# Kernel tuning notes

Hardware: AMD Instinct MI355X
Metric: run time of the kernel (lower is better)

Reference implementation:

```python
import jax, jax.numpy as jnp
import numpy as np

_N = 262144  # horizon
_n = 64      # state dim
_m = 32      # observation dim


def setup_inputs() -> dict:
    key = jax.random.key(0)
    k1, k2, k3, k4 = jax.random.split(key, 4)
    # Scale so the closed-loop matrix M = A - L H is stable (spectral radius < 1);
    # otherwise the 262k-step recurrence overflows fp32.
    A = jax.random.normal(k1, (_n, _n), jnp.float32) * (0.7 / np.sqrt(_n))
    H = jax.random.normal(k2, (_m, _n), jnp.float32) * (1.0 / np.sqrt(_n))
    L = jax.random.normal(k3, (_n, _m), jnp.float32) * (0.1 / np.sqrt(_m))
    y = jax.random.normal(k4, (_m, _N), jnp.float32)
    return {"y": y, "A": A, "H": H, "L": L, "N": _N}


def reference(y, A, H, L, N):
    # xhat[k+1] = A xhat[k] + L (y[:,k] - H xhat[:,k]) = (A - L H) xhat[k] + L y[:,k]
    # yhat[:,k] = H xhat[:,k],  xhat[0] = 0
    M = A - L @ H  # (n, n) closed-loop transition
    x0 = jnp.zeros((A.shape[0],), dtype=A.dtype)

    def step(x, yk):
        yhat_k = H @ x          # emitted BEFORE the update (matches loop order)
        x_next = M @ x + L @ yk
        return x_next, yhat_k

    _, yhat = jax.lax.scan(step, x0, y.T[:N])  # yhat: (N, m)
    return yhat.T  # (m, N)
```

## Files before the change

### kernel.cpp

```cpp
#include <hip/hip_runtime.h>
#include <hip/hip_bf16.h>


#define NSTEP 262144
#define T 16
#define CCH (NSTEP / T)
#define KDIM (64 + 32 * T)
#define MOUT (32 * T)
#define NBLK 128
#define SB (CCH / NBLK)

typedef _Float16 f16;
typedef _Float16 f16x4 __attribute__((ext_vector_type(4)));
typedef _Float16 f16x8 __attribute__((ext_vector_type(8)));
typedef float f32x4 __attribute__((ext_vector_type(4)));


#define OFF_ZH 0
#define SZ_ZH  (CCH * KDIM / 2)
#define OFF_VT (OFF_ZH + SZ_ZH)
#define SZ_VT  (CCH * 64)
#define OFF_MP (OFF_VT + SZ_VT)
#define SZ_MP  (8 * 4096)
#define OFF_BO (OFF_MP + SZ_MP)
#define SZ_BO  (MOUT * KDIM / 2)
#define OFF_GC (OFF_BO + SZ_BO)
#define SZ_GC  (64 * 512 / 2)
#define OFF_FB (OFF_GC + SZ_GC)
#define SZ_FB  (16 * 2048)
#define OFF_GB (OFF_FB + SZ_FB)
#define SZ_GB  (16 * 2048)
#define OFF_KD (OFF_GB + SZ_GB)
#define SZ_KD  (15 * 1024)
#define OFF_W  (OFF_KD + SZ_KD)
#define OFF_XB (OFF_W + NBLK * 64)

__global__ __launch_bounds__(256) void k_pack(const float* __restrict__ y,
                                              f16* __restrict__ Zt) {
  __shared__ f16 Lt[32][264];
  const int tid = threadIdx.x;
  const int ct = blockIdx.x;
  const size_t colbase = (size_t)ct * 256;
#pragma unroll
  for (int v = 0; v < 8; ++v) {
    const int fidx = v * 256 + tid;
    const int row = fidx >> 6, col4 = fidx & 63;
    const float4 w = *reinterpret_cast<const float4*>(y + (size_t)row * NSTEP + colbase + col4 * 4);
    f16x4 h = {(f16)w.x, (f16)w.y, (f16)w.z, (f16)w.w};
    *reinterpret_cast<f16x4*>(&Lt[row][col4 * 4]) = h;
  }
  __syncthreads();
#pragma unroll
  for (int v = 0; v < 4; ++v) {
    const int s = v * 256 + tid;
    const int l = s & 15, lg = (s >> 4) & 3, t = s >> 6;
    f16x8 hv;
#pragma unroll
    for (int e = 0; e < 8; ++e) hv[e] = Lt[lg * 8 + e][l * 16 + t];
    *reinterpret_cast<f16x8*>(Zt + ((size_t)(ct * 18 + 2 + t) * 64 + lg * 16 + l) * 8) = hv;
  }
}

__global__ __launch_bounds__(1024) void k_p1(const float* __restrict__ A,
                                             const float* __restrict__ H,
                                             const float* __restrict__ L,
                                             float* __restrict__ MP,
                                             float* __restrict__ Fb,
                                             float* __restrict__ Gb) {
  __shared__ float B0[64 * 68], B1[64 * 68], B2[64 * 68];
  const int tid = threadIdx.x;
  const int i = tid >> 4;
  const int j0 = (tid & 15) << 2;

  auto mm = [&](float* ldst, const float* X, const float* Y, float* gdst) {
    float c0 = 0.f, c1 = 0.f, c2 = 0.f, c3 = 0.f;
    for (int k = 0; k < 64; ++k) {
      const float r = X[i * 68 + k];
      const float* col = &Y[k * 68 + j0];
      c0 = fmaf(r, col[0], c0); c1 = fmaf(r, col[1], c1);
      c2 = fmaf(r, col[2], c2); c3 = fmaf(r, col[3], c3);
    }
    if (ldst) { ldst[i * 68 + j0 + 0] = c0; ldst[i * 68 + j0 + 1] = c1;
                ldst[i * 68 + j0 + 2] = c2; ldst[i * 68 + j0 + 3] = c3; }
    if (gdst) { gdst[i * 64 + j0 + 0] = c0; gdst[i * 64 + j0 + 1] = c1;
                gdst[i * 64 + j0 + 2] = c2; gdst[i * 64 + j0 + 3] = c3; }
  };

  float a0 = A[i * 64 + j0 + 0], a1 = A[i * 64 + j0 + 1];
  float a2 = A[i * 64 + j0 + 2], a3 = A[i * 64 + j0 + 3];
  for (int q = 0; q < 32; ++q) {
    const float l = L[i * 32 + q];
    a0 -= l * H[q * 64 + j0 + 0]; a1 -= l * H[q * 64 + j0 + 1];
    a2 -= l * H[q * 64 + j0 + 2]; a3 -= l * H[q * 64 + j0 + 3];
  }
  B0[i * 68 + j0 + 0] = a0; B0[i * 68 + j0 + 1] = a1;
  B0[i * 68 + j0 + 2] = a2; B0[i * 68 + j0 + 3] = a3;
  MP[i * 64 + j0 + 0] = a0; MP[i * 64 + j0 + 1] = a1;
  MP[i * 64 + j0 + 2] = a2; MP[i * 64 + j0 + 3] = a3;
  for (int e = tid; e < 2048; e += 1024) { Fb[e] = H[e]; Gb[e] = L[e]; }
  __syncthreads();

  mm(B1, B0, B0, MP + 1 * 4096); __syncthreads();
  mm(nullptr, B1, B0, MP + 6 * 4096); __syncthreads();
  mm(B2, B1, B1, MP + 2 * 4096); __syncthreads();
  mm(B0, B2, B2, MP + 3 * 4096); __syncthreads();
  mm(nullptr, B2, B0, MP + 7 * 4096); __syncthreads();
  mm(B1, B0, B0, MP + 4 * 4096); __syncthreads();
  float* cur = B1; float* oth = B2;
  for (int s2 = 0; s2 < 7; ++s2) {
    mm(oth, cur, cur, (s2 == 6) ? MP + 5 * 4096 : nullptr);
    __syncthreads();
    float* tmp = cur; cur = oth; oth = tmp;
  }
}

__global__ __launch_bounds__(256) void k_fg(const float* __restrict__ MP,
                                            float* __restrict__ Fb,
                                            float* __restrict__ Gb,
                                            const int phase) {
  const int tid = threadIdx.x;
  const int nHalf = phase ? 12 : 3;
  const int half = blockIdx.x / nHalf, r = blockIdx.x % nHalf;
  int src, dst, msl;
  if (phase == 0) { src = 0; dst = r + 1; msl = (r == 0) ? 0 : (r == 1) ? 1 : 6; }
  else { const int b = r / 4 + 1, s = r % 4; src = s; dst = 4 * b + s;
         msl = (b == 1) ? 2 : (b == 2) ? 3 : 7; }
  const float* __restrict__ Mx = MP + msl * 4096;
  if (half == 0) {
    const int j = tid & 63, ih = tid >> 6;
    const float* Fs = Fb + src * 2048;
    float* Fd = Fb + dst * 2048;
#pragma unroll
    for (int u = 0; u < 8; ++u) {
      const int i = ih * 8 + u;
      float acc = 0.f;
#pragma unroll 8
      for (int q = 0; q < 64; ++q) acc = fmaf(Fs[i * 64 + q], Mx[q * 64 + j], acc);
      Fd[i * 64 + j] = acc;
    }
  } else {
    const int q = tid & 31, ih = tid >> 5;
    const float* Gs = Gb + src * 2048;
    float* Gd = Gb + dst * 2048;
#pragma unroll
    for (int u = 0; u < 8; ++u) {
      const int i = ih * 8 + u;
      float acc = 0.f;
#pragma unroll 8
      for (int p = 0; p < 64; ++p) acc = fmaf(Mx[i * 64 + p], Gs[p * 32 + q], acc);
      Gd[i * 32 + q] = acc;
    }
  }
}

__global__ __launch_bounds__(256) void k_kd(const float* __restrict__ Fb,
                                            const float* __restrict__ L,
                                            float* __restrict__ Kd) {
  const int o = blockIdx.x * 256 + threadIdx.x;
  const int d = o >> 10, i = (o >> 5) & 31, q = o & 31;
  float acc = 0.f;
#pragma unroll 8
  for (int j = 0; j < 64; ++j) acc = fmaf(Fb[d * 2048 + i * 64 + j], L[j * 32 + q], acc);
  Kd[o] = acc;
}

__global__ __launch_bounds__(256) void k_asm(const float* __restrict__ Fb,
                                             const float* __restrict__ Gb,
                                             const float* __restrict__ Kd,
                                             f16* __restrict__ BOt,
                                             f16* __restrict__ GCt) {
  const int sid = blockIdx.x * 256 + threadIdx.x;
  if (sid < 512 * 72) {
    const int l = sid & 15, lg = (sid >> 4) & 3;
    const int t18 = sid >> 6;
    const int mt = t18 / 18, ks = t18 - mt * 18;
    const int i = mt, t = l;
    const int k0 = ks * 32 + lg * 8;
    f16x8 hv;
    if (k0 + 7 < 64) {
#pragma unroll
      for (int e = 0; e < 8; ++e) hv[e] = (f16)Fb[t * 2048 + i * 64 + k0 + e];
    } else {
      const int kk = k0 - 64;
      const int s = kk >> 5, q0 = kk & 31;
      if (s < t) {
        const int d = t - 1 - s;
#pragma unroll
        for (int e = 0; e < 8; ++e) hv[e] = (f16)Kd[d * 1024 + i * 32 + q0 + e];
      } else {
#pragma unroll
        for (int e = 0; e < 8; ++e) hv[e] = (f16)0.f;
      }
    }
    *reinterpret_cast<f16x8*>(BOt + (size_t)sid * 8) = hv;
  } else {
    const int sid2 = sid - 512 * 72;
    if (sid2 < 4096) {
      const int l = sid2 & 15, lg = (sid2 >> 4) & 3;
      const int t16 = sid2 >> 6;
      const int jt = t16 >> 4, ks = t16 & 15;
      const int j = jt * 16 + l;
      const int ii = lg * 8;
      f16x8 hv;
#pragma unroll
      for (int e = 0; e < 8; ++e) hv[e] = (f16)Gb[(15 - ks) * 2048 + j * 32 + ii + e];
      *reinterpret_cast<f16x8*>(GCt + (size_t)sid2 * 8) = hv;
    }
  }
}

template <int MODE>
__global__ __launch_bounds__(256) void k_mfma(const f16* __restrict__ At,
                                              const f16* __restrict__ Bt,
                                              float* __restrict__ outp) {
  constexpr int KSTEPS = MODE ? 18 : 16;
  constexpr int AKS0 = MODE ? 0 : 2;
  constexpr int KSB = MODE ? 18 : 16;
  const int tid = threadIdx.x;
  const int wave = tid >> 6, lane = tid & 63;
  const int l15 = lane & 15, lg = lane >> 4;
  const int nn0 = blockIdx.x * 128;
  const int ct0 = blockIdx.x * 8 + wave * 2;
  const int bt0 = MODE ? blockIdx.y * 4 : 0;
  const int laneoff = (lg * 16 + l15) * 8;
  f32x4 acc[2][4] = {};
#pragma unroll 2
  for (int su = 0; su < KSTEPS; ++su) {
    const f16x8 a0 = *reinterpret_cast<const f16x8*>(At + (size_t)((ct0 + 0) * 18 + AKS0 + su) * 512 + laneoff);
    const f16x8 a1 = *reinterpret_cast<const f16x8*>(At + (size_t)((ct0 + 1) * 18 + AKS0 + su) * 512 + laneoff);
#pragma unroll
    for (int bf = 0; bf < 4; ++bf) {
      const f16x8 b = *reinterpret_cast<const f16x8*>(Bt + (size_t)((bt0 + bf) * KSB + su) * 512 + laneoff);
      acc[0][bf] = __builtin_amdgcn_mfma_f32_16x16x32_f16(a0, b, acc[0][bf], 0, 0, 0);
      acc[1][bf] = __builtin_amdgcn_mfma_f32_16x16x32_f16(a1, b, acc[1][bf], 0, 0, 0);
    }
  }
#pragma unroll
  for (int af = 0; af < 2; ++af)
#pragma unroll
    for (int bf = 0; bf < 4; ++bf)
#pragma unroll
      for (int rg = 0; rg < 4; ++rg) {
        const int c = nn0 + wave * 32 + af * 16 + lg * 4 + rg;
        const int mm = bt0 * 16 + bf * 16 + l15;
        if (MODE) {
          outp[(size_t)(mm >> 4) * NSTEP + (size_t)c * 16 + (mm & 15)] = acc[af][bf][rg];
        } else {
          outp[(size_t)c * 64 + mm] = acc[af][bf][rg];
        }
      }
}

__device__ __forceinline__ float lane_bcast(float v, int l) {
  return __uint_as_float(__builtin_amdgcn_readlane(__float_as_uint(v), l));
}

__device__ __forceinline__ float matvec_dot(const float* __restrict__ Prow, float x) {
  float a0 = 0.f, a1 = 0.f, a2 = 0.f, a3 = 0.f;
#pragma unroll
  for (int j = 0; j < 16; ++j) {
    a0 = fmaf(Prow[j +  0], lane_bcast(x, j +  0), a0);
    a1 = fmaf(Prow[j + 16], lane_bcast(x, j + 16), a1);
    a2 = fmaf(Prow[j + 32], lane_bcast(x, j + 32), a2);
    a3 = fmaf(Prow[j + 48], lane_bcast(x, j + 48), a3);
  }
  return (a0 + a1) + (a2 + a3);
}

__device__ __forceinline__ void stage_lds(const float* __restrict__ g,
                                          float* __restrict__ lds,
                                          int n, int lane) {
  const int iters = n >> 8;
  for (int r = 0; r < iters; r += 8) {
    float4 tmp[8];
#pragma unroll
    for (int u = 0; u < 8; ++u)
      tmp[u] = *reinterpret_cast<const float4*>(g + (size_t)(r + u) * 256 + lane * 4);
#pragma unroll
    for (int u = 0; u < 8; ++u)
      *reinterpret_cast<float4*>(lds + (size_t)(r + u) * 256 + lane * 4) = tmp[u];
  }
}

__global__ __launch_bounds__(64, 1) void k_scanA(const float* __restrict__ MP,
                                                 const float* __restrict__ VT,
                                                 float* __restrict__ W) {
  __shared__ float SV[SB * 64];
  const int lane = threadIdx.x;
  const int b = blockIdx.x;
  stage_lds(VT + (size_t)b * SB * 64, SV, SB * 64, lane);
  const float* P = MP + 4 * 4096;
  float Prow[64];
#pragma unroll
  for (int j = 0; j < 64; ++j) Prow[j] = P[lane * 64 + j];
  __syncthreads();
  float x = 0.f;
  for (int s = 0; s < SB; ++s) {
    const float v = SV[s * 64 + lane];
    x = matvec_dot(Prow, x) + v;
  }
  W[b * 64 + lane] = x;
}

__global__ __launch_bounds__(64, 1) void k_scanB(const float* __restrict__ MP,
                                                 const float* __restrict__ W,
                                                 float* __restrict__ XB) {
  __shared__ float SW[NBLK * 64];
  const int lane = threadIdx.x;
  stage_lds(W, SW, NBLK * 64, lane);
  const float* Q = MP + 5 * 4096;
  float Qrow[64];
#pragma unroll
  for (int j = 0; j < 64; ++j) Qrow[j] = Q[lane * 64 + j];
  __syncthreads();
  float x = 0.f;
  for (int b = 0; b < NBLK; ++b) {
    XB[b * 64 + lane] = x;
    const float v = SW[b * 64 + lane];
    x = matvec_dot(Qrow, x) + v;
  }
}

__global__ __launch_bounds__(64, 1) void k_scanC(const float* __restrict__ MP,
                                                 const float* __restrict__ VT,
                                                 const float* __restrict__ XB,
                                                 f16* __restrict__ Zt) {
  __shared__ float SV[SB * 64];
  __shared__ float xt2[SB][68];
  const int lane = threadIdx.x;
  const int b = blockIdx.x;
  stage_lds(VT + (size_t)b * SB * 64, SV, SB * 64, lane);
  const float* P = MP + 4 * 4096;
  float Prow[64];
#pragma unroll
  for (int j = 0; j < 64; ++j) Prow[j] = P[lane * 64 + j];
  float x = XB[b * 64 + lane];
  __syncthreads();
  for (int s = 0; s < SB; ++s) {
    xt2[s][lane] = x;
    const float v = SV[s * 64 + lane];
    x = matvec_dot(Prow, x) + v;
  }
  __syncthreads();
#pragma unroll
  for (int h = 0; h < 2; ++h) {
    const int s = h * 64 + lane;
    const int c = b * SB + s;
    const int ct = c >> 4, l = c & 15;
#pragma unroll
    for (int ks = 0; ks < 2; ++ks)
#pragma unroll
      for (int lg = 0; lg < 4; ++lg) {
        f16x8 hv;
#pragma unroll
        for (int e = 0; e < 8; ++e) hv[e] = (f16)xt2[s][ks * 32 + lg * 8 + e];
        *reinterpret_cast<f16x8*>(Zt + ((size_t)(ct * 18 + ks) * 64 + lg * 16 + l) * 8) = hv;
      }
  }
}

extern "C" void kernel_launch(void* const* d_in, const int* in_sizes, int n_in,
                              void* d_out, int out_size, void* d_ws, size_t ws_size,
                              hipStream_t stream) {
  const float* y = (const float*)d_in[0];
  const float* A = (const float*)d_in[1];
  const float* H = (const float*)d_in[2];
  const float* L = (const float*)d_in[3];
  float* ws = (float*)d_ws;
  f16* Zt   = reinterpret_cast<f16*>(ws + OFF_ZH);
  float* VT = ws + OFF_VT;
  float* MP = ws + OFF_MP;
  f16* BOt  = reinterpret_cast<f16*>(ws + OFF_BO);
  f16* GCt  = reinterpret_cast<f16*>(ws + OFF_GC);
  float* Fb = ws + OFF_FB;
  float* Gb = ws + OFF_GB;
  float* Kd = ws + OFF_KD;
  float* W  = ws + OFF_W;
  float* XB = ws + OFF_XB;
  float* out = (float*)d_out;

  k_pack<<<dim3(CCH / 16), dim3(256), 0, stream>>>(y, Zt);
  k_p1<<<dim3(1), dim3(1024), 0, stream>>>(A, H, L, MP, Fb, Gb);
  k_fg<<<dim3(6), dim3(256), 0, stream>>>(MP, Fb, Gb, 0);
  k_fg<<<dim3(24), dim3(256), 0, stream>>>(MP, Fb, Gb, 1);
  k_kd<<<dim3(60), dim3(256), 0, stream>>>(Fb, L, Kd);
  k_asm<<<dim3(160), dim3(256), 0, stream>>>(Fb, Gb, Kd, BOt, GCt);
  k_mfma<0><<<dim3(CCH / 128, 1), dim3(256), 0, stream>>>(Zt, GCt, VT);
  k_scanA<<<dim3(NBLK), dim3(64), 0, stream>>>(MP, VT, W);
  k_scanB<<<dim3(1), dim3(64), 0, stream>>>(MP, W, XB);
  k_scanC<<<dim3(NBLK), dim3(64), 0, stream>>>(MP, VT, XB, Zt);
  k_mfma<1><<<dim3(CCH / 128, MOUT / 64), dim3(256), 0, stream>>>(Zt, BOt, out);
}
```

Measured before the change: 285.7 us.

## Register-tile setup matmuls and move M^(16·2^7) squaring into first MFMA launch

The single-block setup kernel now uses 128 threads with an 8x4 register-tiled fp32 matmul, so it issues fewer LDS reads and fewer barriers. The seven repeated squarings that produce the highest matrix power are moved out of the serial setup kernel. They now run in one extra block appended to the first MFMA GEMM launch, where they overlap with the GEMM work. That power is only consumed by the later scan kernels. The extra block can lengthen the tail of that launch, and the MFMA kernel now carries a special-case branch.

After: 292.8 us. 1.02x slower.

```diff
diff --git a/kernel.cpp b/kernel.cpp
--- a/kernel.cpp
+++ b/kernel.cpp
@@ -35,6 +35,39 @@
 #define OFF_W  (OFF_KD + SZ_KD)
 #define OFF_XB (OFF_W + NBLK * 64)
 
+__device__ __forceinline__ void mm128(const float* __restrict__ X,
+                                      const float* __restrict__ Y,
+                                      float* __restrict__ D,
+                                      float* __restrict__ gdst,
+                                      const int tid) {
+  const int i0 = (tid >> 4) * 8, j0 = (tid & 15) * 4;
+  float acc[8][4] = {};
+  for (int k0 = 0; k0 < 64; k0 += 4) {
+    float4 yc[4];
+#pragma unroll
+    for (int kk = 0; kk < 4; ++kk)
+      yc[kk] = *reinterpret_cast<const float4*>(&Y[(k0 + kk) * 68 + j0]);
+#pragma unroll
+    for (int r = 0; r < 8; ++r) {
+      const float4 xr = *reinterpret_cast<const float4*>(&X[(i0 + r) * 68 + k0]);
+      const float xs[4] = {xr.x, xr.y, xr.z, xr.w};
+#pragma unroll
+      for (int kk = 0; kk < 4; ++kk) {
+        acc[r][0] = fmaf(xs[kk], yc[kk].x, acc[r][0]);
+        acc[r][1] = fmaf(xs[kk], yc[kk].y, acc[r][1]);
+        acc[r][2] = fmaf(xs[kk], yc[kk].z, acc[r][2]);
+        acc[r][3] = fmaf(xs[kk], yc[kk].w, acc[r][3]);
+      }
+    }
+  }
+#pragma unroll
+  for (int r = 0; r < 8; ++r) {
+    const float4 v = make_float4(acc[r][0], acc[r][1], acc[r][2], acc[r][3]);
+    if (D) *reinterpret_cast<float4*>(&D[(i0 + r) * 68 + j0]) = v;
+    if (gdst) *reinterpret_cast<float4*>(&gdst[(i0 + r) * 64 + j0]) = v;
+  }
+}
+
 __global__ __launch_bounds__(256) void k_pack(const float* __restrict__ y,
                                               f16* __restrict__ Zt) {
   __shared__ f16 Lt[32][264];
@@ -61,57 +94,68 @@
   }
 }
 
-__global__ __launch_bounds__(1024) void k_p1(const float* __restrict__ A,
-                                             const float* __restrict__ H,
-                                             const float* __restrict__ L,
-                                             float* __restrict__ MP,
-                                             float* __restrict__ Fb,
-                                             float* __restrict__ Gb) {
-  __shared__ float B0[64 * 68], B1[64 * 68], B2[64 * 68];
+__global__ __launch_bounds__(128) void k_p1(const float* __restrict__ A,
+                                            const float* __restrict__ H,
+                                            const float* __restrict__ L,
+                                            float* __restrict__ MP,
+                                            float* __restrict__ Fb,
+                                            float* __restrict__ Gb) {
+  __shared__ __align__(16) float S0[64 * 68], S1[64 * 68], S2[64 * 68];
   const int tid = threadIdx.x;
-  const int i = tid >> 4;
-  const int j0 = (tid & 15) << 2;
-
-  auto mm = [&](float* ldst, const float* X, const float* Y, float* gdst) {
-    float c0 = 0.f, c1 = 0.f, c2 = 0.f, c3 = 0.f;
-    for (int k = 0; k < 64; ++k) {
-      const float r = X[i * 68 + k];
-      const float* col = &Y[k * 68 + j0];
-      c0 = fmaf(r, col[0], c0); c1 = fmaf(r, col[1], c1);
-      c2 = fmaf(r, col[2], c2); c3 = fmaf(r, col[3], c3);
-    }
-    if (ldst) { ldst[i * 68 + j0 + 0] = c0; ldst[i * 68 + j0 + 1] = c1;
-                ldst[i * 68 + j0 + 2] = c2; ldst[i * 68 + j0 + 3] = c3; }
-    if (gdst) { gdst[i * 64 + j0 + 0] = c0; gdst[i * 64 + j0 + 1] = c1;
-                gdst[i * 64 + j0 + 2] = c2; gdst[i * 64 + j0 + 3] = c3; }
-  };
-
-  float a0 = A[i * 64 + j0 + 0], a1 = A[i * 64 + j0 + 1];
-  float a2 = A[i * 64 + j0 + 2], a3 = A[i * 64 + j0 + 3];
-  for (int q = 0; q < 32; ++q) {
-    const float l = L[i * 32 + q];
-    a0 -= l * H[q * 64 + j0 + 0]; a1 -= l * H[q * 64 + j0 + 1];
-    a2 -= l * H[q * 64 + j0 + 2]; a3 -= l * H[q * 64 + j0 + 3];
-  }
-  B0[i * 68 + j0 + 0] = a0; B0[i * 68 + j0 + 1] = a1;
-  B0[i * 68 + j0 + 2] = a2; B0[i * 68 + j0 + 3] = a3;
-  MP[i * 64 + j0 + 0] = a0; MP[i * 64 + j0 + 1] = a1;
-  MP[i * 64 + j0 + 2] = a2; MP[i * 64 + j0 + 3] = a3;
-  for (int e = tid; e < 2048; e += 1024) { Fb[e] = H[e]; Gb[e] = L[e]; }
-  __syncthreads();
-
-  mm(B1, B0, B0, MP + 1 * 4096); __syncthreads();
-  mm(nullptr, B1, B0, MP + 6 * 4096); __syncthreads();
-  mm(B2, B1, B1, MP + 2 * 4096); __syncthreads();
-  mm(B0, B2, B2, MP + 3 * 4096); __syncthreads();
-  mm(nullptr, B2, B0, MP + 7 * 4096); __syncthreads();
-  mm(B1, B0, B0, MP + 4 * 4096); __syncthreads();
-  float* cur = B1; float* oth = B2;
-  for (int s2 = 0; s2 < 7; ++s2) {
-    mm(oth, cur, cur, (s2 == 6) ? MP + 5 * 4096 : nullptr);
+  for (int e = tid; e < 512; e += 128) {
+    const float4 v = reinterpret_cast<const float4*>(H)[e];
+    const int q = e >> 4, j = (e & 15) << 2;
+    *reinterpret_cast<float4*>(&S0[q * 68 + j]) = v;
+  }
+  for (int e = tid; e < 512; e += 128) {
+    const float4 v = reinterpret_cast<const float4*>(L)[e];
+    const int i = e >> 3, q = (e & 7) << 2;
+    S1[(q + 0) * 68 + i] = v.x;
+    S1[(q + 1) * 68 + i] = v.y;
+    S1[(q + 2) * 68 + i] = v.z;
+    S1[(q + 3) * 68 + i] = v.w;
+  }
+  for (int e = tid; e < 512; e += 128) {
+    reinterpret_cast<float4*>(Fb)[e] = reinterpret_cast<const float4*>(H)[e];
+    reinterpret_cast<float4*>(Gb)[e] = reinterpret_cast<const float4*>(L)[e];
+  }
+  __syncthreads();
+  {
+    const int i0 = (tid >> 4) * 8, j0 = (tid & 15) * 4;
+    float acc[8][4];
+#pragma unroll
+    for (int r = 0; r < 8; ++r) {
+      const float4 a = *reinterpret_cast<const float4*>(&A[(i0 + r) * 64 + j0]);
+      acc[r][0] = a.x; acc[r][1] = a.y; acc[r][2] = a.z; acc[r][3] = a.w;
+    }
+    for (int q = 0; q < 32; ++q) {
+      const float4 hq = *reinterpret_cast<const float4*>(&S0[q * 68 + j0]);
+      const float4 l0 = *reinterpret_cast<const float4*>(&S1[q * 68 + i0]);
+      const float4 l1 = *reinterpret_cast<const float4*>(&S1[q * 68 + i0 + 4]);
+      const float ls[8] = {l0.x, l0.y, l0.z, l0.w, l1.x, l1.y, l1.z, l1.w};
+#pragma unroll
+      for (int r = 0; r < 8; ++r) {
+        acc[r][0] = fmaf(-ls[r], hq.x, acc[r][0]);
+        acc[r][1] = fmaf(-ls[r], hq.y, acc[r][1]);
+        acc[r][2] = fmaf(-ls[r], hq.z, acc[r][2]);
+        acc[r][3] = fmaf(-ls[r], hq.w, acc[r][3]);
+      }
+    }
     __syncthreads();
-    float* tmp = cur; cur = oth; oth = tmp;
-  }
+#pragma unroll
+    for (int r = 0; r < 8; ++r) {
+      const float4 v = make_float4(acc[r][0], acc[r][1], acc[r][2], acc[r][3]);
+      *reinterpret_cast<float4*>(&S2[(i0 + r) * 68 + j0]) = v;
+      *reinterpret_cast<float4*>(&MP[(i0 + r) * 64 + j0]) = v;
+    }
+  }
+  __syncthreads();
+  mm128(S2, S2, S0, MP + 1 * 4096, tid); __syncthreads();
+  mm128(S0, S2, nullptr, MP + 6 * 4096, tid); __syncthreads();
+  mm128(S0, S0, S1, MP + 2 * 4096, tid); __syncthreads();
+  mm128(S1, S1, S0, MP + 3 * 4096, tid); __syncthreads();
+  mm128(S1, S0, nullptr, MP + 7 * 4096, tid); __syncthreads();
+  mm128(S0, S0, nullptr, MP + 4 * 4096, tid);
 }
 
 __global__ __launch_bounds__(256) void k_fg(const float* __restrict__ MP,
@@ -212,7 +256,25 @@
 template <int MODE>
 __global__ __launch_bounds__(256) void k_mfma(const f16* __restrict__ At,
                                               const f16* __restrict__ Bt,
-                                              float* __restrict__ outp) {
+                                              float* __restrict__ outp,
+                                              float* __restrict__ MPow) {
+  if (MODE == 0 && blockIdx.x == CCH / 128) {
+    __shared__ __align__(16) float C0[64 * 68], C1[64 * 68];
+    const int tid2 = threadIdx.x;
+    const float* M16 = MPow + 4 * 4096;
+    for (int e = tid2; e < 4096; e += 256)
+      C0[(e >> 6) * 68 + (e & 63)] = M16[e];
+    __syncthreads();
+    float* cur = C0;
+    float* nxt = C1;
+    for (int s = 0; s < 7; ++s) {
+      if (tid2 < 128)
+        mm128(cur, cur, nxt, (s == 6) ? (MPow + 5 * 4096) : nullptr, tid2);
+      __syncthreads();
+      float* t = cur; cur = nxt; nxt = t;
+    }
+    return;
+  }
   constexpr int KSTEPS = MODE ? 18 : 16;
   constexpr int AKS0 = MODE ? 0 : 2;
   constexpr int KSB = MODE ? 18 : 16;
@@ -380,14 +442,14 @@
   float* out = (float*)d_out;
 
   k_pack<<<dim3(CCH / 16), dim3(256), 0, stream>>>(y, Zt);
-  k_p1<<<dim3(1), dim3(1024), 0, stream>>>(A, H, L, MP, Fb, Gb);
+  k_p1<<<dim3(1), dim3(128), 0, stream>>>(A, H, L, MP, Fb, Gb);
   k_fg<<<dim3(6), dim3(256), 0, stream>>>(MP, Fb, Gb, 0);
   k_fg<<<dim3(24), dim3(256), 0, stream>>>(MP, Fb, Gb, 1);
   k_kd<<<dim3(60), dim3(256), 0, stream>>>(Fb, L, Kd);
   k_asm<<<dim3(160), dim3(256), 0, stream>>>(Fb, Gb, Kd, BOt, GCt);
-  k_mfma<0><<<dim3(CCH / 128, 1), dim3(256), 0, stream>>>(Zt, GCt, VT);
+  k_mfma<0><<<dim3(CCH / 128 + 1, 1), dim3(256), 0, stream>>>(Zt, GCt, VT, MP);
   k_scanA<<<dim3(NBLK), dim3(64), 0, stream>>>(MP, VT, W);
   k_scanB<<<dim3(1), dim3(64), 0, stream>>>(MP, W, XB);
   k_scanC<<<dim3(NBLK), dim3(64), 0, stream>>>(MP, VT, XB, Zt);
-  k_mfma<1><<<dim3(CCH / 128, MOUT / 64), dim3(256), 0, stream>>>(Zt, BOt, out);
-}
+  k_mfma<1><<<dim3(CCH / 128, MOUT / 64), dim3(256), 0, stream>>>(Zt, BOt, out, nullptr);
+}
```
